# Performance work log

Measured on AMD Instinct MI355X. Metric: run time of the kernel, lower is better.

Reference implementation:

```python
import jax, jax.numpy as jnp
import numpy as np

M, NQ, NK = 2, 1024, 1024
DX, DT = 256, 2
H, D = 8, 32          # num_heads, head_dim
KH = 32               # kernel MLP hidden width
SCALE = D ** -0.5


def setup_inputs() -> dict:
    key = jax.random.key(0)
    ks = jax.random.split(key, 16)
    p = 0.02
    return {
        "xq": jax.random.normal(ks[0], (M, NQ, DX), jnp.float32),
        "xk": jax.random.normal(ks[1], (M, NK, DX), jnp.float32),
        "xv": jax.random.normal(ks[2], (M, NK, DX), jnp.float32),
        "tq": jax.random.normal(ks[3], (M, NQ, DT), jnp.float32),
        "tk": jax.random.normal(ks[4], (M, NK, DT), jnp.float32),
        # projections (no bias, as in nn.Linear(..., bias=False))
        "Wq": jax.random.normal(ks[5], (DX, H * D), jnp.float32) * p,
        "Wk": jax.random.normal(ks[6], (DX, H * D), jnp.float32) * p,
        "Wv": jax.random.normal(ks[7], (DX, H * D), jnp.float32) * p,
        # output projection (with bias)
        "Wo": jax.random.normal(ks[8], (H * D, DX), jnp.float32) * p,
        "bo": jnp.zeros((DX,), jnp.float32),
        # kernel MLP: dt -> KH -> H
        "Wk1": jax.random.normal(ks[9], (DT, KH), jnp.float32) * 0.5,
        "bk1": jnp.zeros((KH,), jnp.float32),
        "Wk2": jax.random.normal(ks[10], (KH, H), jnp.float32) * 0.5,
        "bk2": jnp.zeros((H,), jnp.float32),
        # phi_t: H -> DT
        "Wphi": jax.random.normal(ks[11], (H, DT), jnp.float32) * p,
        "bphi": jnp.zeros((DT,), jnp.float32),
    }


def reference(xq, xk, xv, tq, tk, Wq, Wk, Wv, Wo, bo, Wk1, bk1, Wk2, bk2, Wphi, bphi):
    m, nq, _ = xq.shape
    nk = xk.shape[1]
    # translation group action: diff [m, nq, nk, dt]
    diff = tq[:, :, None, :] - tk[:, None, :, :]
    # q, k: [m, h, n, d]
    q = (xq @ Wq).reshape(m, nq, H, D).transpose(0, 2, 1, 3)
    k = (xk @ Wk).reshape(m, nk, H, D).transpose(0, 2, 1, 3)
    token_dots = jnp.einsum("bhqd,bhkd->bhqk", q, k) * SCALE
    # kernel MLP bias evaluated densely over diffs -> [m, nq, nk, h] -> [m, h, nq, nk]
    hdn = jax.nn.relu(diff @ Wk1 + bk1)
    kdots = (hdn @ Wk2 + bk2).transpose(0, 3, 1, 2)
    dots = kdots + token_dots
    attn = jax.nn.softmax(dots, axis=-1)  # [m, h, nq, nk]
    v = (xv @ Wv).reshape(m, nk, H, D).transpose(0, 2, 1, 3)
    out = jnp.einsum("bhqk,bhkd->bhqd", attn, v)
    out = out.transpose(0, 2, 1, 3).reshape(m, nq, H * D)
    out = out @ Wo + bo  # dropout p=0
    # phi_t path: attn -> [m, nq, nk, h] -> per-pair dt weights
    attn_t = attn.transpose(0, 2, 3, 1)
    t_dots = attn_t @ Wphi + bphi  # [m, nq, nk, dt]
    tq_new = tq + (1.0 / nk) * jnp.sum(diff * t_dots, axis=-2)
    return out, tq_new
```

## Files before the change

kernel.cpp:

```cpp
#include <hip/hip_runtime.h>
#include <hip/hip_bf16.h>

#define MB 2
#define NQ 1024
#define NK 1024
#define DXC 256
#define HD 256
#define HH 8
#define DD 32
#define KHC 32
#define LOG2E 1.4426950408889634f
#define QSCALE 0.25503472301046627f

#define QB 32
#define KB 32
#define KSPLIT 8
#define KL 128
#define NCHUNK 4

#define QPB_F   0u
#define KPB_F   262144u
#define VPT_F   524288u
#define WT_F    786432u
#define AQH_F   917504u
#define BKH_F   950272u
#define TS_F    983040u
#define TKX_F   983048u
#define W2T_F   986120u
#define PART_F  986376u

typedef float f32x4 __attribute__((ext_vector_type(4)));
typedef short bf16x8 __attribute__((ext_vector_type(8)));
typedef _Float16 f16x8 __attribute__((ext_vector_type(8)));
typedef _Float16 f16x2 __attribute__((ext_vector_type(2)));

#define MFMA(a, b, c)   __builtin_amdgcn_mfma_f32_16x16x32_bf16(a, b, c, 0, 0, 0)
#define MFMA16(a, b, c) __builtin_amdgcn_mfma_f32_16x16x32_f16(a, b, c, 0, 0, 0)
#define EXP2(x) exp2f(x)

#define KDQ 36
#define KDH 1160
#define SMEM_BYTES 28800

struct Ptrs {
    const float *xq, *xk, *xv, *tq, *tk;
    const float *Wq, *Wk, *Wv, *Wo, *bo;
    const float *Wk1, *bk1, *Wk2, *bk2, *Wphi, *bphi;
    float* wsf;
    float* out;
};

__device__ __forceinline__ uint cvt_pk_bf16(float lo, float hi) {
    uint r;
    asm("v_cvt_pk_bf16_f32 %0, %1, %2" : "=v"(r) : "v"(lo), "v"(hi));
    return r;
}
__device__ __forceinline__ ushort f2bf1(float f) { return (ushort)cvt_pk_bf16(f, 0.f); }
__device__ __forceinline__ float bf2f(uint x) {
    return __uint_as_float((x & 0xffffu) << 16);
}
__device__ __forceinline__ ushort f2h(float f) {
    _Float16 h = (_Float16)f;
    return __builtin_bit_cast(ushort, h);
}

__device__ __forceinline__ void phase1(int u, int t, const Ptrs& p, char* smem_raw) {
    ushort* wt  = (ushort*)(p.wsf + WT_F);
    ushort* aqh = (ushort*)(p.wsf + AQH_F);
    ushort* bkh = (ushort*)(p.wsf + BKH_F);
    ushort* tkx = (ushort*)(p.wsf + TKX_F);
    ushort* w2t = (ushort*)(p.wsf + W2T_F);
    float*  ts  = p.wsf + TS_F;

    if (u < 64) {
        const int mat = u >> 4;
        const float* W = (mat == 0) ? p.Wq : (mat == 1) ? p.Wk : (mat == 2) ? p.Wv : p.Wo;
        const int k0 = (u & 3) * 64, c0 = ((u >> 2) & 3) * 64;
        float (*sW)[65] = (float(*)[65])smem_raw;
        #pragma unroll
        for (int i = 0; i < 4; ++i) {
            int flat = i * 1024 + t * 4;
            int r = flat >> 6, c = flat & 63;
            float4 v4 = *(const float4*)(W + (size_t)(k0 + r) * 256 + c0 + c);
            sW[r][c] = v4.x; sW[r][c + 1] = v4.y; sW[r][c + 2] = v4.z; sW[r][c + 3] = v4.w;
        }
        __syncthreads();
        #pragma unroll
        for (int i = 0; i < 4; ++i) {
            int flat = i * 1024 + t * 4;
            int cc = flat >> 6, kk = flat & 63;
            uint2 pk;
            pk.x = cvt_pk_bf16(sW[kk][cc], sW[kk + 1][cc]);
            pk.y = cvt_pk_bf16(sW[kk + 2][cc], sW[kk + 3][cc]);
            *(uint2*)(wt + (size_t)mat * 65536 + (size_t)(c0 + cc) * 256 + k0 + kk) = pk;
        }
    } else if (u < 320) {
        int gid = (u - 64) * 256 + t;
        int row = gid >> 5, j = gid & 31;
        aqh[gid] = f2h(p.tq[row * 2] * p.Wk1[j] + p.tq[row * 2 + 1] * p.Wk1[KHC + j] + p.bk1[j]);
        bkh[gid] = f2h(p.tk[row * 2] * p.Wk1[j] + p.tk[row * 2 + 1] * p.Wk1[KHC + j]);
    } else if (u < 344) {
        int g = (u - 320) * 256 + t;
        int mm = g / 3072, rr = (g % 3072) >> 10, kk = g & 1023;
        float v = (rr == 0) ? p.tk[(size_t)(mm * NK + kk) * 2]
                : (rr == 1) ? p.tk[(size_t)(mm * NK + kk) * 2 + 1] : 1.0f;
        tkx[g] = f2bf1(v);
    } else if (u == 344) {
        for (int g = t; g < 512; g += 256) {
            int hh2 = g >> 5, jj = g & 31;
            w2t[g] = f2h(hh2 < HH ? p.Wk2[jj * HH + hh2] * LOG2E : 0.f);
        }
    } else {
        const int m = u - 345;
        const int c = t & 1, kk = t >> 1;
        float s = 0.f;
        #pragma unroll
        for (int i = 0; i < 8; ++i) s += p.tk[(size_t)(m * NK + kk + i * 128) * 2 + c];
        float* red = (float*)smem_raw;
        red[t] = s; __syncthreads();
        for (int off = 128; off >= 2; off >>= 1) {
            if (t < off) red[t] += red[t + off];
            __syncthreads();
        }
        if (t < 2) ts[m * 2 + t] = red[t];
    }
}

__device__ __forceinline__ void phase2(int u, int t, const Ptrs& p, char* smem_raw) {
    ushort* qpb = (ushort*)(p.wsf + QPB_F);
    ushort* kpb = (ushort*)(p.wsf + KPB_F);
    ushort* vpt = (ushort*)(p.wsf + VPT_F);
    const ushort* wt = (const ushort*)(p.wsf + WT_F);

    const int z = u / 128;
    const int R0 = (u % 128) * 16;
    const float* x = (z == 0) ? p.xq : (z == 1) ? p.xk : p.xv;
    const ushort* wz = wt + (size_t)z * 65536;
    const int wid = t >> 6, l = t & 63, g = l >> 4, c16 = l & 15;
    const int wc = wid * 64;
    const int row = R0 + c16;

    f32x4 acc[4];
    #pragma unroll
    for (int i = 0; i < 4; ++i) acc[i] = (f32x4){0.f, 0.f, 0.f, 0.f};

    for (int k0 = 0; k0 < DXC; k0 += 32) {
        const float* xr = x + (size_t)row * DXC + k0 + g * 8;
        float4 a0 = *(const float4*)xr;
        float4 a1 = *(const float4*)(xr + 4);
        union { bf16x8 v; uint d[4]; } af;
        af.d[0] = cvt_pk_bf16(a0.x, a0.y);
        af.d[1] = cvt_pk_bf16(a0.z, a0.w);
        af.d[2] = cvt_pk_bf16(a1.x, a1.y);
        af.d[3] = cvt_pk_bf16(a1.z, a1.w);
        #pragma unroll
        for (int cf = 0; cf < 4; ++cf) {
            bf16x8 bf = *(const bf16x8*)(wz + (size_t)(wc + cf * 16 + c16) * 256 + k0 + g * 8);
            acc[cf] = MFMA(af.v, bf, acc[cf]);
        }
    }
    if (z != 2) {
        #pragma unroll
        for (int cf = 0; cf < 4; ++cf) {
            #pragma unroll
            for (int r = 0; r < 4; ++r) {
                int orow = R0 + g * 4 + r;
                int col = wc + cf * 16 + c16;
                float v = acc[cf][r];
                if (z == 0) qpb[(size_t)orow * HD + col] = f2bf1(v * QSCALE);
                else        kpb[(size_t)orow * HD + col] = f2bf1(v);
            }
        }
    } else {
        ushort (*sTr)[24] = (ushort(*)[24])smem_raw;
        #pragma unroll
        for (int cf = 0; cf < 4; ++cf)
            #pragma unroll
            for (int r = 0; r < 4; ++r)
                sTr[wc + cf * 16 + c16][g * 4 + r] = f2bf1(acc[cf][r]);
        __syncthreads();
        const int mq = R0 >> 10, rin = R0 & 1023;
        ushort* dst = vpt + (size_t)mq * (HD * NK) + (size_t)t * NK + rin;
        *(uint4*)dst       = *(const uint4*)&sTr[t][0];
        *(uint4*)(dst + 8) = *(const uint4*)&sTr[t][8];
    }
}

__device__ __forceinline__ void phase3(int u, int t, const Ptrs& p, char* smem_raw) {
    const ushort* qpb = (const ushort*)(p.wsf + QPB_F);
    const ushort* kpb = (const ushort*)(p.wsf + KPB_F);
    const ushort* vpt = (const ushort*)(p.wsf + VPT_F);
    const ushort* aqh = (const ushort*)(p.wsf + AQH_F);
    const ushort* bkh = (const ushort*)(p.wsf + BKH_F);
    const ushort* tkx = (const ushort*)(p.wsf + TKX_F);
    const ushort* w2t = (const ushort*)(p.wsf + W2T_F);
    ushort* part = (ushort*)(p.wsf + PART_F);

    const int ks = u & 7;
    const int qt = (u >> 3) & 31;
    const int m  = u >> 8;
    const int q0 = qt * QB;
    const int kbase = ks * KL;
    const int wid = t >> 6;
    const int l = t & 63;
    const int g = l >> 4;
    const int c16 = l & 15;

    ushort* sKD = (ushort*)smem_raw;
    ushort (*sP)[32][40] = (ushort(*)[32][40])(smem_raw + 18560);

    f16x8 w2v = *(const f16x8*)(w2t + c16 * 32 + g * 8);
    const float b2l = (c16 < HH) ? p.bk2[c16] * LOG2E : 0.f;
    const f16x8 zero8 = {0, 0, 0, 0, 0, 0, 0, 0};

    bf16x8 qb[2][2];
    #pragma unroll
    for (int hh = 0; hh < 2; ++hh)
        #pragma unroll
        for (int qf = 0; qf < 2; ++qf)
            qb[hh][qf] = *(const bf16x8*)(qpb + (size_t)(m * NQ + q0 + qf * 16 + c16) * HD
                                              + (wid * 2 + hh) * DD + g * 8);
    f16x8 aqv[8];
    #pragma unroll
    for (int qi = 0; qi < 8; ++qi)
        aqv[qi] = *(const f16x8*)(aqh + (size_t)(m * NQ + q0 + wid * 8 + qi) * KHC + g * 8);

    f32x4 oacc[2][2][3];
    #pragma unroll
    for (int a = 0; a < 2; ++a)
        #pragma unroll
        for (int bb = 0; bb < 2; ++bb)
            #pragma unroll
            for (int c = 0; c < 3; ++c)
                oacc[a][bb][c] = (f32x4){0.f, 0.f, 0.f, 0.f};

    for (int ch = 0; ch < NCHUNK; ++ch) {
        const int k0 = kbase + ch * KB;
        {
            f16x8 bkf0 = *(const f16x8*)(bkh + (size_t)(m * NK + k0 + c16) * KHC + g * 8);
            f16x8 bkf1 = *(const f16x8*)(bkh + (size_t)(m * NK + k0 + 16 + c16) * KHC + g * 8);
            #pragma unroll
            for (int qi = 0; qi < 8; ++qi) {
                const int q = wid * 8 + qi;
                #pragma unroll
                for (int kh = 0; kh < 2; ++kh) {
                    f16x8 d = aqv[qi] - (kh ? bkf1 : bkf0);
                    f16x8 hv = __builtin_elementwise_max(d, zero8);
                    f32x4 c = {b2l, b2l, b2l, b2l};
                    c = MFMA16(hv, w2v, c);
                    if (c16 < HH) {
                        uint2 st;
                        st.x = __builtin_bit_cast(uint, __builtin_amdgcn_cvt_pkrtz(c[0], c[1]));
                        st.y = __builtin_bit_cast(uint, __builtin_amdgcn_cvt_pkrtz(c[2], c[3]));
                        *(uint2*)&sKD[c16 * KDH + q * KDQ + kh * 16 + g * 4] = st;
                    }
                }
            }
        }
        __syncthreads();

        #pragma unroll
        for (int hh = 0; hh < 2; ++hh) {
            const int h = wid * 2 + hh;
            bf16x8 ka0 = *(const bf16x8*)(kpb + (size_t)(m * NK + k0 + c16) * HD + h * DD + g * 8);
            bf16x8 ka1 = *(const bf16x8*)(kpb + (size_t)(m * NK + k0 + 16 + c16) * HD + h * DD + g * 8);
            const ushort* kdb = &sKD[h * KDH];
            #pragma unroll
            for (int kf = 0; kf < 2; ++kf) {
                #pragma unroll
                for (int qf = 0; qf < 2; ++qf) {
                    uint2 kd2 = *(const uint2*)&kdb[(qf * 16 + c16) * KDQ + kf * 16 + g * 4];
                    f16x2 k01 = __builtin_bit_cast(f16x2, kd2.x);
                    f16x2 k23 = __builtin_bit_cast(f16x2, kd2.y);
                    f32x4 cinit = {(float)k01[0], (float)k01[1], (float)k23[0], (float)k23[1]};
                    f32x4 s = MFMA((kf ? ka1 : ka0), qb[hh][qf], cinit);
                    uint2 pk;
                    pk.x = cvt_pk_bf16(EXP2(s[0]), EXP2(s[1]));
                    pk.y = cvt_pk_bf16(EXP2(s[2]), EXP2(s[3]));
                    *(uint2*)&sP[wid][qf * 16 + c16][kf * 16 + g * 4] = pk;
                }
            }
            bf16x8 vb0 = *(const bf16x8*)(vpt + (size_t)m * (HD * NK) + (size_t)(h * DD + c16) * NK + k0 + g * 8);
            bf16x8 vb1 = *(const bf16x8*)(vpt + (size_t)m * (HD * NK) + (size_t)(h * DD + 16 + c16) * NK + k0 + g * 8);
            bf16x8 vbt = *(const bf16x8*)(tkx + (size_t)m * 3072 + (size_t)(c16 < 2 ? c16 : 2) * NK + k0 + g * 8);
            #pragma unroll
            for (int qf = 0; qf < 2; ++qf) {
                bf16x8 pa = *(const bf16x8*)&sP[wid][qf * 16 + c16][g * 8];
                oacc[hh][qf][0] = MFMA(pa, vb0, oacc[hh][qf][0]);
                oacc[hh][qf][1] = MFMA(pa, vb1, oacc[hh][qf][1]);
                oacc[hh][qf][2] = MFMA(pa, vbt, oacc[hh][qf][2]);
            }
        }
        __syncthreads();
    }

    #pragma unroll
    for (int hh = 0; hh < 2; ++hh) {
        int mh = m * HH + wid * 2 + hh;
        #pragma unroll
        for (int qf = 0; qf < 2; ++qf) {
            #pragma unroll
            for (int r = 0; r < 4; ++r) {
                int q = q0 + qf * 16 + g * 4 + r;
                ushort* pb = part + ((size_t)(mh * KSPLIT + ks) * NQ + q) * 40;
                pb[c16]      = f2bf1(oacc[hh][qf][0][r]);
                pb[16 + c16] = f2bf1(oacc[hh][qf][1][r]);
                float e = oacc[hh][qf][2][r];
                if (c16 < 2) pb[32 + c16] = f2bf1(e);
                else if (c16 == 2) *(float*)(pb + 34) = e;
            }
        }
    }
}

__device__ __forceinline__ void phase4(int u, int t, const Ptrs& p, char* smem_raw) {
    const ushort* part = (const ushort*)(p.wsf + PART_F);
    const ushort* wt = (const ushort*)(p.wsf + WT_F);
    const float* ts = p.wsf + TS_F;
    float* tq_out = p.out + (size_t)MB * NQ * HD;

    ushort (*sHob)[264] = (ushort(*)[264])smem_raw;
    float (*sD)[16][2] = (float(*)[16][2])(smem_raw + 8448);
    const int m = u >> 6;
    const int q0 = (u & 63) * 16;
    const int h = t >> 5, dgrp = (t >> 4) & 1, qloc = t & 15;
    const int q = q0 + qloc;
    const int mh = m * HH + h;

    float accO[16] = {};
    float aT = 0.f, lsum = 0.f;
    for (int s = 0; s < KSPLIT; ++s) {
        const ushort* ps = part + ((size_t)(mh * KSPLIT + s) * NQ + q) * 40;
        uint4 v0 = *(const uint4*)(ps + dgrp * 16);
        uint4 v1 = *(const uint4*)(ps + dgrp * 16 + 8);
        accO[0] += bf2f(v0.x); accO[1] += bf2f(v0.x >> 16);
        accO[2] += bf2f(v0.y); accO[3] += bf2f(v0.y >> 16);
        accO[4] += bf2f(v0.z); accO[5] += bf2f(v0.z >> 16);
        accO[6] += bf2f(v0.w); accO[7] += bf2f(v0.w >> 16);
        accO[8] += bf2f(v1.x); accO[9] += bf2f(v1.x >> 16);
        accO[10] += bf2f(v1.y); accO[11] += bf2f(v1.y >> 16);
        accO[12] += bf2f(v1.z); accO[13] += bf2f(v1.z >> 16);
        accO[14] += bf2f(v1.w); accO[15] += bf2f(v1.w >> 16);
        uint at = *(const uint*)(ps + 32);
        aT += bf2f(dgrp == 0 ? at : (at >> 16));
        lsum += *(const float*)(ps + 34);
    }
    const float inv = 1.f / lsum;
    {
        uint dd[8];
        #pragma unroll
        for (int i = 0; i < 8; ++i)
            dd[i] = cvt_pk_bf16(accO[2 * i] * inv, accO[2 * i + 1] * inv);
        ushort* hp = &sHob[qloc][h * DD + dgrp * 16];
        *(uint4*)hp       = (uint4){dd[0], dd[1], dd[2], dd[3]};
        *(uint4*)(hp + 8) = (uint4){dd[4], dd[5], dd[6], dd[7]};
    }
    const float A = aT * inv;
    const float tqc = p.tq[(size_t)(m * NQ + q) * 2 + dgrp];
    sD[h][qloc][dgrp] = p.Wphi[h * 2 + dgrp] * (tqc - A);
    __syncthreads();

    if (t < 32) {
        int ql2 = t >> 1, c = t & 1;
        float s = 0.f;
        #pragma unroll
        for (int hh2 = 0; hh2 < 8; ++hh2) s += sD[hh2][ql2][c];
        int qg = q0 + ql2;
        float tqv = p.tq[(size_t)(m * NQ + qg) * 2 + c];
        const float invnk = 1.f / (float)NK;
        tq_out[(size_t)(m * NQ + qg) * 2 + c] =
            tqv + s * invnk + p.bphi[c] * (tqv - ts[m * 2 + c] * invnk);
    }

    const ushort* wz3 = wt + (size_t)3 * 65536;
    const int wid = t >> 6, l = t & 63, g = l >> 4, c16 = l & 15;
    f32x4 acc[4];
    #pragma unroll
    for (int i = 0; i < 4; ++i) acc[i] = (f32x4){0.f, 0.f, 0.f, 0.f};
    for (int k0 = 0; k0 < HD; k0 += 32) {
        bf16x8 af = *(const bf16x8*)&sHob[c16][k0 + g * 8];
        #pragma unroll
        for (int cf = 0; cf < 4; ++cf) {
            int col = wid * 64 + cf * 16 + c16;
            bf16x8 bf = *(const bf16x8*)(wz3 + (size_t)col * 256 + k0 + g * 8);
            acc[cf] = MFMA(af, bf, acc[cf]);
        }
    }
    #pragma unroll
    for (int cf = 0; cf < 4; ++cf) {
        int col = wid * 64 + cf * 16 + c16;
        float bv = p.bo[col];
        #pragma unroll
        for (int r = 0; r < 4; ++r) {
            int orow = q0 + g * 4 + r;
            p.out[(size_t)(m * NQ + orow) * DXC + col] = acc[cf][r] + bv;
        }
    }
}

__global__ __launch_bounds__(256, 4) void k_phase1(Ptrs p) {
    __shared__ __align__(16) char smem[SMEM_BYTES];
    phase1(blockIdx.x, threadIdx.x, p, smem);
}
__global__ __launch_bounds__(256, 4) void k_phase2(Ptrs p) {
    __shared__ __align__(16) char smem[SMEM_BYTES];
    phase2(blockIdx.x, threadIdx.x, p, smem);
}
__global__ __launch_bounds__(256, 4) void k_phase3(Ptrs p) {
    __shared__ __align__(16) char smem[SMEM_BYTES];
    phase3(blockIdx.x, threadIdx.x, p, smem);
}
__global__ __launch_bounds__(256, 4) void k_phase4(Ptrs p) {
    __shared__ __align__(16) char smem[SMEM_BYTES];
    phase4(blockIdx.x, threadIdx.x, p, smem);
}

extern "C" void kernel_launch(void* const* d_in, const int* in_sizes, int n_in,
                              void* d_out, int out_size, void* d_ws, size_t ws_size,
                              hipStream_t stream)
{
    Ptrs p;
    p.xq   = (const float*)d_in[0];
    p.xk   = (const float*)d_in[1];
    p.xv   = (const float*)d_in[2];
    p.tq   = (const float*)d_in[3];
    p.tk   = (const float*)d_in[4];
    p.Wq   = (const float*)d_in[5];
    p.Wk   = (const float*)d_in[6];
    p.Wv   = (const float*)d_in[7];
    p.Wo   = (const float*)d_in[8];
    p.bo   = (const float*)d_in[9];
    p.Wk1  = (const float*)d_in[10];
    p.bk1  = (const float*)d_in[11];
    p.Wk2  = (const float*)d_in[12];
    p.bk2  = (const float*)d_in[13];
    p.Wphi = (const float*)d_in[14];
    p.bphi = (const float*)d_in[15];
    p.wsf  = (float*)d_ws;
    p.out  = (float*)d_out;

    hipLaunchKernelGGL(k_phase1, dim3(347), dim3(256), 0, stream, p);
    hipLaunchKernelGGL(k_phase2, dim3(384), dim3(256), 0, stream, p);
    hipLaunchKernelGGL(k_phase3, dim3(512), dim3(256), 0, stream, p);
    hipLaunchKernelGGL(k_phase4, dim3(128), dim3(256), 0, stream, p);
}
```

Baseline: 62.67 us.

## Prefetch next K/V chunk into registers in attention phase and right-size shared memory

In the attention kernel, the global loads of the K, V, kernel-MLP bias and tk operands for the next chunk are issued before computing the current chunk. This double-buffers them in registers to hide load latency. Launch bounds for that kernel drop from 4 to 2 blocks per CU so the extra registers fit, at the cost of fewer resident waves. The other phase kernels now declare only the shared memory they use instead of a common maximum, which can raise their occupancy.

After: 56.90 us. 9.2% less time.

```diff
diff --git a/kernel.cpp b/kernel.cpp
--- a/kernel.cpp
+++ b/kernel.cpp
@@ -64,7 +64,10 @@
     return __builtin_bit_cast(ushort, h);
 }
 
-__device__ __forceinline__ void phase1(int u, int t, const Ptrs& p, char* smem_raw) {
+__global__ __launch_bounds__(256, 4) void k_phase1(Ptrs p) {
+    __shared__ __align__(16) float sW[64][65];
+    const int u = blockIdx.x;
+    const int t = threadIdx.x;
     ushort* wt  = (ushort*)(p.wsf + WT_F);
     ushort* aqh = (ushort*)(p.wsf + AQH_F);
     ushort* bkh = (ushort*)(p.wsf + BKH_F);
@@ -76,7 +79,6 @@
         const int mat = u >> 4;
         const float* W = (mat == 0) ? p.Wq : (mat == 1) ? p.Wk : (mat == 2) ? p.Wv : p.Wo;
         const int k0 = (u & 3) * 64, c0 = ((u >> 2) & 3) * 64;
-        float (*sW)[65] = (float(*)[65])smem_raw;
         #pragma unroll
         for (int i = 0; i < 4; ++i) {
             int flat = i * 1024 + t * 4;
@@ -116,7 +118,7 @@
         float s = 0.f;
         #pragma unroll
         for (int i = 0; i < 8; ++i) s += p.tk[(size_t)(m * NK + kk + i * 128) * 2 + c];
-        float* red = (float*)smem_raw;
+        float* red = (float*)&sW[0][0];
         red[t] = s; __syncthreads();
         for (int off = 128; off >= 2; off >>= 1) {
             if (t < off) red[t] += red[t + off];
@@ -126,7 +128,10 @@
     }
 }
 
-__device__ __forceinline__ void phase2(int u, int t, const Ptrs& p, char* smem_raw) {
+__global__ __launch_bounds__(256, 4) void k_phase2(Ptrs p) {
+    __shared__ __align__(16) ushort sTr[256][24];
+    const int u = blockIdx.x;
+    const int t = threadIdx.x;
     ushort* qpb = (ushort*)(p.wsf + QPB_F);
     ushort* kpb = (ushort*)(p.wsf + KPB_F);
     ushort* vpt = (ushort*)(p.wsf + VPT_F);
@@ -172,7 +177,6 @@
             }
         }
     } else {
-        ushort (*sTr)[24] = (ushort(*)[24])smem_raw;
         #pragma unroll
         for (int cf = 0; cf < 4; ++cf)
             #pragma unroll
@@ -186,7 +190,11 @@
     }
 }
 
-__device__ __forceinline__ void phase3(int u, int t, const Ptrs& p, char* smem_raw) {
+__global__ __launch_bounds__(256, 2) void k_phase3(Ptrs p) {
+    __shared__ __align__(16) char smem[SMEM_BYTES];
+    const int u = blockIdx.x;
+    const int t = threadIdx.x;
+
     const ushort* qpb = (const ushort*)(p.wsf + QPB_F);
     const ushort* kpb = (const ushort*)(p.wsf + KPB_F);
     const ushort* vpt = (const ushort*)(p.wsf + VPT_F);
@@ -206,8 +214,8 @@
     const int g = l >> 4;
     const int c16 = l & 15;
 
-    ushort* sKD = (ushort*)smem_raw;
-    ushort (*sP)[32][40] = (ushort(*)[32][40])(smem_raw + 18560);
+    ushort* sKD = (ushort*)smem;
+    ushort (*sP)[32][40] = (ushort(*)[32][40])(smem + 18560);
 
     f16x8 w2v = *(const f16x8*)(w2t + c16 * 32 + g * 8);
     const float b2l = (c16 < HH) ? p.bk2[c16] * LOG2E : 0.f;
@@ -225,6 +233,29 @@
     for (int qi = 0; qi < 8; ++qi)
         aqv[qi] = *(const f16x8*)(aqh + (size_t)(m * NQ + q0 + wid * 8 + qi) * KHC + g * 8);
 
+    struct ChunkOps {
+        f16x8 bk0, bk1;
+        bf16x8 ka0[2], ka1[2], v0[2], v1[2];
+        bf16x8 vt;
+    };
+    const size_t vbase = (size_t)m * (HD * NK);
+    const size_t tbase = (size_t)m * 3072 + (size_t)(c16 < 2 ? c16 : 2) * NK;
+    auto loadChunk = [&](int k0) {
+        ChunkOps c;
+        c.bk0 = *(const f16x8*)(bkh + (size_t)(m * NK + k0 + c16) * KHC + g * 8);
+        c.bk1 = *(const f16x8*)(bkh + (size_t)(m * NK + k0 + 16 + c16) * KHC + g * 8);
+        #pragma unroll
+        for (int hh = 0; hh < 2; ++hh) {
+            const int h = wid * 2 + hh;
+            c.ka0[hh] = *(const bf16x8*)(kpb + (size_t)(m * NK + k0 + c16) * HD + h * DD + g * 8);
+            c.ka1[hh] = *(const bf16x8*)(kpb + (size_t)(m * NK + k0 + 16 + c16) * HD + h * DD + g * 8);
+            c.v0[hh]  = *(const bf16x8*)(vpt + vbase + (size_t)(h * DD + c16) * NK + k0 + g * 8);
+            c.v1[hh]  = *(const bf16x8*)(vpt + vbase + (size_t)(h * DD + 16 + c16) * NK + k0 + g * 8);
+        }
+        c.vt = *(const bf16x8*)(tkx + tbase + k0 + g * 8);
+        return c;
+    };
+
     f32x4 oacc[2][2][3];
     #pragma unroll
     for (int a = 0; a < 2; ++a)
@@ -234,17 +265,18 @@
             for (int c = 0; c < 3; ++c)
                 oacc[a][bb][c] = (f32x4){0.f, 0.f, 0.f, 0.f};
 
+    ChunkOps cur = loadChunk(kbase);
     for (int ch = 0; ch < NCHUNK; ++ch) {
-        const int k0 = kbase + ch * KB;
+        ChunkOps nxt;
+        if (ch + 1 < NCHUNK) nxt = loadChunk(kbase + (ch + 1) * KB);
+
         {
-            f16x8 bkf0 = *(const f16x8*)(bkh + (size_t)(m * NK + k0 + c16) * KHC + g * 8);
-            f16x8 bkf1 = *(const f16x8*)(bkh + (size_t)(m * NK + k0 + 16 + c16) * KHC + g * 8);
             #pragma unroll
             for (int qi = 0; qi < 8; ++qi) {
                 const int q = wid * 8 + qi;
                 #pragma unroll
                 for (int kh = 0; kh < 2; ++kh) {
-                    f16x8 d = aqv[qi] - (kh ? bkf1 : bkf0);
+                    f16x8 d = aqv[qi] - (kh ? cur.bk1 : cur.bk0);
                     f16x8 hv = __builtin_elementwise_max(d, zero8);
                     f32x4 c = {b2l, b2l, b2l, b2l};
                     c = MFMA16(hv, w2v, c);
@@ -262,8 +294,6 @@
         #pragma unroll
         for (int hh = 0; hh < 2; ++hh) {
             const int h = wid * 2 + hh;
-            bf16x8 ka0 = *(const bf16x8*)(kpb + (size_t)(m * NK + k0 + c16) * HD + h * DD + g * 8);
-            bf16x8 ka1 = *(const bf16x8*)(kpb + (size_t)(m * NK + k0 + 16 + c16) * HD + h * DD + g * 8);
             const ushort* kdb = &sKD[h * KDH];
             #pragma unroll
             for (int kf = 0; kf < 2; ++kf) {
@@ -273,25 +303,23 @@
                     f16x2 k01 = __builtin_bit_cast(f16x2, kd2.x);
                     f16x2 k23 = __builtin_bit_cast(f16x2, kd2.y);
                     f32x4 cinit = {(float)k01[0], (float)k01[1], (float)k23[0], (float)k23[1]};
-                    f32x4 s = MFMA((kf ? ka1 : ka0), qb[hh][qf], cinit);
+                    f32x4 s = MFMA((kf ? cur.ka1[hh] : cur.ka0[hh]), qb[hh][qf], cinit);
                     uint2 pk;
                     pk.x = cvt_pk_bf16(EXP2(s[0]), EXP2(s[1]));
                     pk.y = cvt_pk_bf16(EXP2(s[2]), EXP2(s[3]));
                     *(uint2*)&sP[wid][qf * 16 + c16][kf * 16 + g * 4] = pk;
                 }
             }
-            bf16x8 vb0 = *(const bf16x8*)(vpt + (size_t)m * (HD * NK) + (size_t)(h * DD + c16) * NK + k0 + g * 8);
-            bf16x8 vb1 = *(const bf16x8*)(vpt + (size_t)m * (HD * NK) + (size_t)(h * DD + 16 + c16) * NK + k0 + g * 8);
-            bf16x8 vbt = *(const bf16x8*)(tkx + (size_t)m * 3072 + (size_t)(c16 < 2 ? c16 : 2) * NK + k0 + g * 8);
             #pragma unroll
             for (int qf = 0; qf < 2; ++qf) {
                 bf16x8 pa = *(const bf16x8*)&sP[wid][qf * 16 + c16][g * 8];
-                oacc[hh][qf][0] = MFMA(pa, vb0, oacc[hh][qf][0]);
-                oacc[hh][qf][1] = MFMA(pa, vb1, oacc[hh][qf][1]);
-                oacc[hh][qf][2] = MFMA(pa, vbt, oacc[hh][qf][2]);
+                oacc[hh][qf][0] = MFMA(pa, cur.v0[hh], oacc[hh][qf][0]);
+                oacc[hh][qf][1] = MFMA(pa, cur.v1[hh], oacc[hh][qf][1]);
+                oacc[hh][qf][2] = MFMA(pa, cur.vt, oacc[hh][qf][2]);
             }
         }
         __syncthreads();
+        if (ch + 1 < NCHUNK) cur = nxt;
     }
 
     #pragma unroll
@@ -313,14 +341,16 @@
     }
 }
 
-__device__ __forceinline__ void phase4(int u, int t, const Ptrs& p, char* smem_raw) {
+__global__ __launch_bounds__(256, 4) void k_phase4(Ptrs p) {
+    __shared__ __align__(16) ushort sHob[16][264];
+    __shared__ float sD[8][16][2];
+    const int u = blockIdx.x;
+    const int t = threadIdx.x;
     const ushort* part = (const ushort*)(p.wsf + PART_F);
     const ushort* wt = (const ushort*)(p.wsf + WT_F);
     const float* ts = p.wsf + TS_F;
     float* tq_out = p.out + (size_t)MB * NQ * HD;
 
-    ushort (*sHob)[264] = (ushort(*)[264])smem_raw;
-    float (*sD)[16][2] = (float(*)[16][2])(smem_raw + 8448);
     const int m = u >> 6;
     const int q0 = (u & 63) * 16;
     const int h = t >> 5, dgrp = (t >> 4) & 1, qloc = t & 15;
@@ -396,23 +426,6 @@
             p.out[(size_t)(m * NQ + orow) * DXC + col] = acc[cf][r] + bv;
         }
     }
-}
-
-__global__ __launch_bounds__(256, 4) void k_phase1(Ptrs p) {
-    __shared__ __align__(16) char smem[SMEM_BYTES];
-    phase1(blockIdx.x, threadIdx.x, p, smem);
-}
-__global__ __launch_bounds__(256, 4) void k_phase2(Ptrs p) {
-    __shared__ __align__(16) char smem[SMEM_BYTES];
-    phase2(blockIdx.x, threadIdx.x, p, smem);
-}
-__global__ __launch_bounds__(256, 4) void k_phase3(Ptrs p) {
-    __shared__ __align__(16) char smem[SMEM_BYTES];
-    phase3(blockIdx.x, threadIdx.x, p, smem);
-}
-__global__ __launch_bounds__(256, 4) void k_phase4(Ptrs p) {
-    __shared__ __align__(16) char smem[SMEM_BYTES];
-    phase4(blockIdx.x, threadIdx.x, p, smem);
 }
 
 extern "C" void kernel_launch(void* const* d_in, const int* in_sizes, int n_in,
```
